# Optimization experiments

Hardware: AMD Instinct MI355X
Metric: run time of the kernel (lower is better)

Reference implementation:

```python
import jax, jax.numpy as jnp
import numpy as np

N, E = 50000, 600000
IN_C, HID, OUT_C = 256, 128, 2
R, B, L = 7, 8, 3
ALPHA = 0.1


def _rgcn(x, src, dst, etype, comp, basis, root, bias):
    # comp: [R,B], basis: [B,d,d] -> per-relation weights W: [R,d,d]
    n, d = x.shape
    W = jnp.einsum('rb,bdf->rdf', comp, basis)
    # combined (dst, relation) segment id for per-relation mean aggregation
    seg = dst * R + etype
    msg = x[src]  # [E,d] gather
    s = jax.ops.segment_sum(msg, seg, num_segments=n * R)  # [N*R,d]
    cnt = jax.ops.segment_sum(jnp.ones((E,), x.dtype), seg, num_segments=n * R)
    agg = (s / jnp.maximum(cnt, 1.0)[:, None]).reshape(n, R, d)  # per-relation mean
    return x @ root + bias + jnp.einsum('nrd,rdf->nf', agg, W)


def setup_inputs() -> dict:
    key = jax.random.key(0)
    ks = jax.random.split(key, 10)
    sc = 0.05
    x = jax.random.normal(ks[0], (N, IN_C), dtype=jnp.float32)
    edge_index = jax.random.randint(ks[1], (2, E), 0, N)
    edge_type = jax.random.randint(ks[2], (E,), 0, R)
    # GPR temp init: alpha*(1-alpha)^k, last entry (1-alpha)^K
    temp = jnp.asarray(ALPHA * (1.0 - ALPHA) ** np.arange(L + 1), dtype=jnp.float32)
    temp = temp.at[-1].set((1.0 - ALPHA) ** L)
    lin1_w = jax.random.normal(ks[3], (IN_C, HID), jnp.float32) * sc
    lin1_b = jnp.zeros((HID,), jnp.float32)
    lin2_w = jax.random.normal(ks[4], (HID, OUT_C), jnp.float32) * sc
    lin2_b = jnp.zeros((OUT_C,), jnp.float32)
    comps = jax.random.normal(ks[5], (L, R, B), jnp.float32) * sc
    bases = jax.random.normal(ks[6], (L, B, HID, HID), jnp.float32) * sc
    roots = jax.random.normal(ks[7], (L, HID, HID), jnp.float32) * sc
    conv_biases = jnp.zeros((L, HID), jnp.float32)
    return dict(x=x, edge_index=edge_index, edge_type=edge_type, temp=temp,
                lin1_w=lin1_w, lin1_b=lin1_b, lin2_w=lin2_w, lin2_b=lin2_b,
                comps=comps, bases=bases, roots=roots, conv_biases=conv_biases)


def reference(x, edge_index, edge_type, temp, lin1_w, lin1_b, lin2_w, lin2_b,
              comps, bases, roots, conv_biases):
    src, dst = edge_index[0], edge_index[1]
    h = x @ lin1_w + lin1_b
    hidden = h * temp[0]
    cur = hidden
    for i in range(L):
        cur = _rgcn(cur, src, dst, edge_type, comps[i], bases[i], roots[i], conv_biases[i])
        if i < L - 1:
            cur = jax.nn.relu(cur)  # dropout p=0.4 is identity in eval mode
        hidden = hidden + temp[i + 1] * cur
    return hidden @ lin2_w + lin2_b
```

## Files before the change

### kernel.cpp

```cpp
#include <hip/hip_runtime.h>
#include <cstdint>


constexpr int N_NODES  = 50000;
constexpr int E_EDGES  = 600000;
constexpr int R_REL    = 7;
constexpr int HID      = 128;
constexpr int IN_C     = 256;
constexpr int L_LAYERS = 3;
constexpr int AGG_COLS = 896;
constexpr int K_CAT    = 1024;
constexpr int NR       = N_NODES * R_REL;
constexpr int SCANR_BLOCKS = (NR + 255) / 256;

#define DEVI __device__ __forceinline__

using short8  = __attribute__((ext_vector_type(8))) short;
using floatx4 = __attribute__((ext_vector_type(4))) float;

DEVI unsigned short f2bf(float f) {
  unsigned u = __float_as_uint(f);
  unsigned r = (u + 0x7FFFu + ((u >> 16) & 1u)) >> 16;
  return (unsigned short)r;
}
DEVI float bf2f(unsigned short h) { return __uint_as_float(((unsigned)h) << 16); }

__global__ __launch_bounds__(256) void cast_x_kernel(
    const float* __restrict__ x, unsigned short* __restrict__ xbf)
{
  int i = blockIdx.x * 256 + threadIdx.x;
  if (i >= N_NODES * IN_C / 4) return;
  float4 v = ((const float4*)x)[i];
  uint2 p;
  p.x = (unsigned)f2bf(v.x) | ((unsigned)f2bf(v.y) << 16);
  p.y = (unsigned)f2bf(v.z) | ((unsigned)f2bf(v.w) << 16);
  ((uint2*)xbf)[i] = p;
}

__global__ __launch_bounds__(256) void cast_w1_kernel(
    const float* __restrict__ w1, unsigned short* __restrict__ w1T)
{
  int t = blockIdx.x * 256 + threadIdx.x;
  if (t >= HID * IN_C) return;
  int m = t >> 8, k = t & 255;
  w1T[m * IN_C + k] = f2bf(w1[k * HID + m]);
}

__global__ __launch_bounds__(256) void build_wcat2(
    const float* __restrict__ comps,
    const float* __restrict__ bases,
    const float* __restrict__ roots,
    unsigned short* __restrict__ wcat2T)
{
  int t = blockIdx.x * 256 + threadIdx.x;
  if (t >= L_LAYERS * 128 * K_CAT) return;
  int l   = t >> 17;
  int rem = t & 131071;
  int f   = rem >> 10;
  int k   = rem & 1023;
  float v;
  if (k < 128) {
    v = roots[((size_t)l * 128 + k) * 128 + f];
  } else {
    int r = (k - 128) >> 7, d = (k - 128) & 127;
    const float* cp = comps + ((size_t)l * R_REL + r) * 8;
    const float* bp = bases + (((size_t)l * 8) * 128 + d) * 128 + f;
    float s = 0.f;
#pragma unroll
    for (int b = 0; b < 8; ++b) s += cp[b] * bp[(size_t)b * 128 * 128];
    v = s;
  }
  wcat2T[t] = f2bf(v);
}

__global__ __launch_bounds__(256) void hist_kernel(
    const int* __restrict__ ei, const int* __restrict__ et,
    int* __restrict__ cntRel)
{
  int e = blockIdx.x * 256 + threadIdx.x;
  if (e >= E_EDGES) return;
  atomicAdd(&cntRel[ei[E_EDGES + e] * R_REL + et[e]], 1);
}

__global__ __launch_bounds__(256) void scanA_kernel(
    const int* __restrict__ cnt, int* __restrict__ tmpOff,
    int* __restrict__ blockSums)
{
  __shared__ int s[256];
  int i = blockIdx.x * 256 + threadIdx.x;
  int v = (i < NR) ? cnt[i] : 0;
  s[threadIdx.x] = v;
  __syncthreads();
#pragma unroll
  for (int d = 1; d < 256; d <<= 1) {
    int t = (threadIdx.x >= d) ? s[threadIdx.x - d] : 0;
    __syncthreads();
    s[threadIdx.x] += t;
    __syncthreads();
  }
  if (i < NR) tmpOff[i] = s[threadIdx.x] - v;
  if (threadIdx.x == 255) blockSums[blockIdx.x] = s[255];
}

__global__ __launch_bounds__(256) void scanB_kernel(int* __restrict__ bs)
{
  __shared__ int s[256];
  __shared__ int carry;
  if (threadIdx.x == 0) carry = 0;
  __syncthreads();
  for (int base = 0; base < SCANR_BLOCKS; base += 256) {
    int cOld = carry;
    int i = base + threadIdx.x;
    int v = (i < SCANR_BLOCKS) ? bs[i] : 0;
    s[threadIdx.x] = v;
    __syncthreads();
#pragma unroll
    for (int d = 1; d < 256; d <<= 1) {
      int t = (threadIdx.x >= d) ? s[threadIdx.x - d] : 0;
      __syncthreads();
      s[threadIdx.x] += t;
      __syncthreads();
    }
    if (i < SCANR_BLOCKS) bs[i] = s[threadIdx.x] - v + cOld;
    __syncthreads();
    if (threadIdx.x == 0) carry = cOld + s[255];
    __syncthreads();
  }
}

__global__ __launch_bounds__(256) void scanC_kernel(
    const int* __restrict__ tmpOff, const int* __restrict__ blockSums,
    int* __restrict__ drs)
{
  int i = blockIdx.x * 256 + threadIdx.x;
  if (i < NR) drs[i] = tmpOff[i] + blockSums[blockIdx.x];
  if (i == 0) drs[NR] = E_EDGES;
}

__global__ __launch_bounds__(256) void place_kernel(
    const int* __restrict__ ei, const int* __restrict__ et,
    const int* __restrict__ drs, int* __restrict__ cursor,
    unsigned short* __restrict__ esrc)
{
  int e = blockIdx.x * 256 + threadIdx.x;
  if (e >= E_EDGES) return;
  int seg = ei[E_EDGES + e] * R_REL + et[e];
  int pos = drs[seg] + atomicAdd(&cursor[seg], 1);
  esrc[pos] = (unsigned short)ei[e];
}

__global__ __launch_bounds__(256) void agg_reg_kernel(
    const unsigned short* __restrict__ curA,
    const unsigned short* __restrict__ esrc,
    const int* __restrict__ drs,
    unsigned short* __restrict__ aggB)
{
  const int tid  = threadIdx.x;
  const int lane = tid & 63;
  const int dst  = blockIdx.x * 4 + (tid >> 6);
  if (dst >= N_NODES) return;
  const int segBase = dst * R_REL;

  int bnd = drs[segBase + (lane & 7)];
  const int a0    = __shfl(bnd, 0);
  const int total = __shfl(bnd, 7) - a0;

  int pk = 0;
  if (lane < total) pk = (int)esrc[a0 + lane];

  const unsigned* colp = (const unsigned*)curA + lane;

  int p = a0;
  int aPrev = a0;
#pragma unroll
  for (int r = 0; r < R_REL; ++r) {
    int br = __shfl(bnd, r + 1);
    float sx = 0.f, sy = 0.f;
    for (; p < br; ++p) {
      int idx = p - a0;
      int src = (idx < 64) ? __shfl(pk, idx) : (int)esrc[p];
      unsigned v = colp[src * 64];
      sx += bf2f((unsigned short)(v & 0xFFFF));
      sy += bf2f((unsigned short)(v >> 16));
    }
    int c = br - aPrev;
    float sc = (c > 0) ? 1.0f / (float)c : 0.f;
    unsigned pck = (unsigned)f2bf(sx * sc) | ((unsigned)f2bf(sy * sc) << 16);
    *(unsigned*)(aggB + (size_t)dst * AGG_COLS + r * HID + lane * 2) = pck;
    aPrev = br;
  }
}

__global__ __launch_bounds__(256) void gemm_lin1(
    const unsigned short* __restrict__ A,
    const unsigned short* __restrict__ BT,
    const float* __restrict__ bias,
    const float* __restrict__ temp,
    float* __restrict__ out0,
    unsigned short* __restrict__ outT)
{
  __shared__ unsigned short As[128][136];
  __shared__ unsigned short Bs[128][136];
  const int tid  = threadIdx.x;
  const int row0 = blockIdx.x * 128;
  const int lane = tid & 63;
  const int wid  = tid >> 6;
  const int wrow = (wid & 1) * 64;
  const int wcol = (wid >> 1) * 64;
  const int l15  = lane & 15;
  const int quad = lane >> 4;

  floatx4 acc[4][4] = {};

  for (int k0 = 0; k0 < IN_C; k0 += 128) {
#pragma unroll
    for (int it = 0; it < 8; ++it) {
      int chunk = it * 256 + tid;
      int r = chunk >> 4, cc = (chunk & 15) << 3;
      int grow = row0 + r;
      uint4 va = make_uint4(0u, 0u, 0u, 0u);
      if (grow < N_NODES)
        va = *(const uint4*)(A + (size_t)grow * IN_C + k0 + cc);
      *(uint4*)(&As[r][cc]) = va;
      *(uint4*)(&Bs[r][cc]) = *(const uint4*)(BT + (size_t)r * IN_C + k0 + cc);
    }
    __syncthreads();
#pragma unroll
    for (int ks = 0; ks < 4; ++ks) {
      int kc = ks * 32 + quad * 8;
      short8 af[4], bfr[4];
#pragma unroll
      for (int i = 0; i < 4; ++i)
        af[i] = *(const short8*)(&As[wrow + i * 16 + l15][kc]);
#pragma unroll
      for (int j = 0; j < 4; ++j)
        bfr[j] = *(const short8*)(&Bs[wcol + j * 16 + l15][kc]);
#pragma unroll
      for (int i = 0; i < 4; ++i)
#pragma unroll
        for (int j = 0; j < 4; ++j)
          acc[i][j] = __builtin_amdgcn_mfma_f32_16x16x32_bf16(
              af[i], bfr[j], acc[i][j], 0, 0, 0);
    }
    __syncthreads();
  }

  float t0 = temp[0];
#pragma unroll
  for (int i = 0; i < 4; ++i) {
    int lrow0 = wrow + i * 16 + quad * 4;
#pragma unroll
    for (int j = 0; j < 4; ++j) {
      int gcol = wcol + j * 16 + l15;
      float bb = bias[gcol];
#pragma unroll
      for (int r = 0; r < 4; ++r) {
        float v = t0 * (acc[i][j][r] + bb);
        int grow = row0 + lrow0 + r;
        if (grow < N_NODES) out0[(size_t)grow * HID + gcol] = v;
        As[lrow0 + r][gcol] = f2bf(v);
      }
    }
  }
  __syncthreads();
#pragma unroll
  for (int it = 0; it < 8; ++it) {
    int chunk = it * 256 + tid;
    int r = chunk >> 4, cc = (chunk & 15) << 3;
    int grow = row0 + r;
    if (grow < N_NODES)
      *(uint4*)(outT + (size_t)grow * HID + cc) = *(const uint4*)(&As[r][cc]);
  }
}

__global__ __launch_bounds__(256) void gemm_layer(
    const unsigned short* __restrict__ curA,
    const unsigned short* __restrict__ aggB,
    const unsigned short* __restrict__ BT,
    const float* __restrict__ bias,
    const float* __restrict__ temp,
    float* __restrict__ hidden,
    unsigned short* __restrict__ curAout,
    int layer)
{
  __shared__ unsigned short Atile[64][136];
  __shared__ unsigned short Btile[128][136];
  const int tid  = threadIdx.x;
  const int row0 = blockIdx.x * 64;
  const int lane = tid & 63;
  const int wid  = tid >> 6;
  const int wrow = (wid & 1) * 32;
  const int wcol = (wid >> 1) * 64;
  const int l15  = lane & 15;
  const int quad = lane >> 4;

  floatx4 acc[2][4] = {};

  for (int p = 0; p < 8; ++p) {
#pragma unroll
    for (int it = 0; it < 8; ++it) {
      int chunk = it * 256 + tid;
      int n = chunk >> 4, cc = (chunk & 15) << 3;
      *(uint4*)(&Btile[n][cc]) =
          *(const uint4*)(BT + (size_t)n * K_CAT + p * 128 + cc);
    }
#pragma unroll
    for (int it = 0; it < 4; ++it) {
      int chunk = it * 256 + tid;
      int r = chunk >> 4, cc = (chunk & 15) << 3;
      int grow = row0 + r;
      uint4 va = make_uint4(0u, 0u, 0u, 0u);
      if (grow < N_NODES) {
        if (p == 0)
          va = *(const uint4*)(curA + (size_t)grow * HID + cc);
        else
          va = *(const uint4*)(aggB + (size_t)grow * AGG_COLS +
                               (p - 1) * 128 + cc);
      }
      *(uint4*)(&Atile[r][cc]) = va;
    }
    __syncthreads();
#pragma unroll
    for (int ks = 0; ks < 4; ++ks) {
      int kc = ks * 32 + quad * 8;
      short8 af[2], bfr[4];
#pragma unroll
      for (int i = 0; i < 2; ++i)
        af[i] = *(const short8*)(&Atile[wrow + i * 16 + l15][kc]);
#pragma unroll
      for (int j = 0; j < 4; ++j)
        bfr[j] = *(const short8*)(&Btile[wcol + j * 16 + l15][kc]);
#pragma unroll
      for (int i = 0; i < 2; ++i)
#pragma unroll
        for (int j = 0; j < 4; ++j)
          acc[i][j] = __builtin_amdgcn_mfma_f32_16x16x32_bf16(
              af[i], bfr[j], acc[i][j], 0, 0, 0);
    }
    __syncthreads();
  }

  const float tl = temp[layer + 1];
  const bool isLast = (layer == L_LAYERS - 1);
#pragma unroll
  for (int i = 0; i < 2; ++i) {
    int lrow0 = wrow + i * 16 + quad * 4;
#pragma unroll
    for (int j = 0; j < 4; ++j) {
      int gcol = wcol + j * 16 + l15;
      float bb = bias[gcol];
#pragma unroll
      for (int r = 0; r < 4; ++r) {
        int grow = row0 + lrow0 + r;
        float c = acc[i][j][r] + bb;
        if (!isLast) c = fmaxf(c, 0.f);
        if (grow < N_NODES) {
          float* hp = hidden + (size_t)grow * HID + gcol;
          *hp += tl * c;
        }
        Atile[lrow0 + r][gcol] = f2bf(c);
      }
    }
  }
  if (!isLast) {
    __syncthreads();
#pragma unroll
    for (int it = 0; it < 4; ++it) {
      int chunk = it * 256 + tid;
      int r = chunk >> 4, cc = (chunk & 15) << 3;
      int grow = row0 + r;
      if (grow < N_NODES)
        *(uint4*)(curAout + (size_t)grow * HID + cc) =
            *(const uint4*)(&Atile[r][cc]);
    }
  }
}

__global__ __launch_bounds__(256) void final_kernel(
    const float* __restrict__ hidden, const float* __restrict__ w2,
    const float* __restrict__ b2, float* __restrict__ out)
{
  int node = blockIdx.x * 4 + (threadIdx.x >> 6);
  int lane = threadIdx.x & 63;
  if (node >= N_NODES) return;
  float h0 = hidden[(size_t)node * HID + lane];
  float h1 = hidden[(size_t)node * HID + 64 + lane];
  float a0 = h0 * w2[lane * 2 + 0] + h1 * w2[(lane + 64) * 2 + 0];
  float a1 = h0 * w2[lane * 2 + 1] + h1 * w2[(lane + 64) * 2 + 1];
#pragma unroll
  for (int off = 32; off > 0; off >>= 1) {
    a0 += __shfl_down(a0, off);
    a1 += __shfl_down(a1, off);
  }
  if (lane == 0) {
    out[node * 2 + 0] = a0 + b2[0];
    out[node * 2 + 1] = a1 + b2[1];
  }
}

extern "C" void kernel_launch(void* const* d_in, const int* in_sizes, int n_in,
                              void* d_out, int out_size, void* d_ws, size_t ws_size,
                              hipStream_t stream) {
  const float* x     = (const float*)d_in[0];
  const int*   ei    = (const int*)d_in[1];
  const int*   et    = (const int*)d_in[2];
  const float* temp  = (const float*)d_in[3];
  const float* w1    = (const float*)d_in[4];
  const float* b1    = (const float*)d_in[5];
  const float* w2    = (const float*)d_in[6];
  const float* b2    = (const float*)d_in[7];
  const float* comps = (const float*)d_in[8];
  const float* bases = (const float*)d_in[9];
  const float* roots = (const float*)d_in[10];
  const float* cbias = (const float*)d_in[11];

  char* ws = (char*)d_ws;
  size_t off = 0;
  auto take = [&](size_t bytes) {
    char* p = ws + off;
    off = (off + bytes + 255) & ~(size_t)255;
    return p;
  };
  unsigned short* wcat2T = (unsigned short*)take((size_t)L_LAYERS * 128 * K_CAT * 2);
  unsigned short* xbf    = (unsigned short*)take((size_t)N_NODES * IN_C * 2);
  unsigned short* w1T    = (unsigned short*)take((size_t)HID * IN_C * 2);
  int*   cntRel  = (int*)take((size_t)NR * 4);
  int*   tmpOffR = (int*)take((size_t)NR * 4);
  int*   blockSumsR = (int*)take((size_t)SCANR_BLOCKS * 4);
  int*   drs     = (int*)take((size_t)(NR + 1) * 4);
  int*   cursorR = (int*)take((size_t)NR * 4);
  unsigned short* esrc = (unsigned short*)take((size_t)E_EDGES * 2);
  float* hidden  = (float*)take((size_t)N_NODES * HID * 4);
  unsigned short* curA  = (unsigned short*)take((size_t)N_NODES * HID * 2);
  unsigned short* curA2 = (unsigned short*)take((size_t)N_NODES * HID * 2);
  unsigned short* aggB  = (unsigned short*)take((size_t)N_NODES * AGG_COLS * 2);

  hipMemsetAsync(cntRel, 0, (size_t)NR * 4, stream);
  hipMemsetAsync(cursorR, 0, (size_t)NR * 4, stream);

  hipLaunchKernelGGL(build_wcat2, dim3((L_LAYERS * 128 * K_CAT + 255) / 256),
                     dim3(256), 0, stream, comps, bases, roots, wcat2T);
  hipLaunchKernelGGL(cast_x_kernel, dim3((N_NODES * IN_C / 4 + 255) / 256),
                     dim3(256), 0, stream, x, xbf);
  hipLaunchKernelGGL(cast_w1_kernel, dim3((HID * IN_C + 255) / 256), dim3(256),
                     0, stream, w1, w1T);
  hipLaunchKernelGGL(hist_kernel, dim3((E_EDGES + 255) / 256), dim3(256), 0,
                     stream, ei, et, cntRel);
  hipLaunchKernelGGL(scanA_kernel, dim3(SCANR_BLOCKS), dim3(256), 0, stream,
                     cntRel, tmpOffR, blockSumsR);
  hipLaunchKernelGGL(scanB_kernel, dim3(1), dim3(256), 0, stream, blockSumsR);
  hipLaunchKernelGGL(scanC_kernel, dim3(SCANR_BLOCKS), dim3(256), 0, stream,
                     tmpOffR, blockSumsR, drs);
  hipLaunchKernelGGL(place_kernel, dim3((E_EDGES + 255) / 256), dim3(256), 0,
                     stream, ei, et, drs, cursorR, esrc);

  const int rowBlocks   = (N_NODES + 127) / 128;
  const int rowBlocks64 = (N_NODES + 63) / 64;
  hipLaunchKernelGGL(gemm_lin1, dim3(rowBlocks), dim3(256), 0, stream,
                     xbf, w1T, b1, temp, hidden, curA);

  const unsigned short* cin = curA;
  unsigned short* cout = curA2;
  for (int l = 0; l < L_LAYERS; ++l) {
    hipLaunchKernelGGL(agg_reg_kernel, dim3((N_NODES + 3) / 4), dim3(256),
                       0, stream, cin, esrc, drs, aggB);
    hipLaunchKernelGGL(gemm_layer, dim3(rowBlocks64), dim3(256), 0, stream,
                       cin, aggB, wcat2T + (size_t)l * 128 * K_CAT,
                       cbias + (size_t)l * HID, temp, hidden, cout, l);
    const unsigned short* t = cin; cin = cout; cout = (unsigned short*)t;
  }

  hipLaunchKernelGGL(final_kernel, dim3((N_NODES + 3) / 4), dim3(256), 0, stream,
                     hidden, w2, b2, (float*)d_out);
}
```

Before: 587.7 us.

## Fuse x cast into lin1 GEMM and defer the hidden accumulation to the final kernel

```diff
diff --git a/kernel.cpp b/kernel.cpp
--- a/kernel.cpp
+++ b/kernel.cpp
@@ -24,18 +24,6 @@
   return (unsigned short)r;
 }
 DEVI float bf2f(unsigned short h) { return __uint_as_float(((unsigned)h) << 16); }
-
-__global__ __launch_bounds__(256) void cast_x_kernel(
-    const float* __restrict__ x, unsigned short* __restrict__ xbf)
-{
-  int i = blockIdx.x * 256 + threadIdx.x;
-  if (i >= N_NODES * IN_C / 4) return;
-  float4 v = ((const float4*)x)[i];
-  uint2 p;
-  p.x = (unsigned)f2bf(v.x) | ((unsigned)f2bf(v.y) << 16);
-  p.y = (unsigned)f2bf(v.z) | ((unsigned)f2bf(v.w) << 16);
-  ((uint2*)xbf)[i] = p;
-}
 
 __global__ __launch_bounds__(256) void cast_w1_kernel(
     const float* __restrict__ w1, unsigned short* __restrict__ w1T)
@@ -192,96 +180,11 @@
 }
 
 __global__ __launch_bounds__(256) void gemm_lin1(
-    const unsigned short* __restrict__ A,
+    const float* __restrict__ x,
     const unsigned short* __restrict__ BT,
     const float* __restrict__ bias,
     const float* __restrict__ temp,
-    float* __restrict__ out0,
-    unsigned short* __restrict__ outT)
-{
-  __shared__ unsigned short As[128][136];
-  __shared__ unsigned short Bs[128][136];
-  const int tid  = threadIdx.x;
-  const int row0 = blockIdx.x * 128;
-  const int lane = tid & 63;
-  const int wid  = tid >> 6;
-  const int wrow = (wid & 1) * 64;
-  const int wcol = (wid >> 1) * 64;
-  const int l15  = lane & 15;
-  const int quad = lane >> 4;
-
-  floatx4 acc[4][4] = {};
-
-  for (int k0 = 0; k0 < IN_C; k0 += 128) {
-#pragma unroll
-    for (int it = 0; it < 8; ++it) {
-      int chunk = it * 256 + tid;
-      int r = chunk >> 4, cc = (chunk & 15) << 3;
-      int grow = row0 + r;
-      uint4 va = make_uint4(0u, 0u, 0u, 0u);
-      if (grow < N_NODES)
-        va = *(const uint4*)(A + (size_t)grow * IN_C + k0 + cc);
-      *(uint4*)(&As[r][cc]) = va;
-      *(uint4*)(&Bs[r][cc]) = *(const uint4*)(BT + (size_t)r * IN_C + k0 + cc);
-    }
-    __syncthreads();
-#pragma unroll
-    for (int ks = 0; ks < 4; ++ks) {
-      int kc = ks * 32 + quad * 8;
-      short8 af[4], bfr[4];
-#pragma unroll
-      for (int i = 0; i < 4; ++i)
-        af[i] = *(const short8*)(&As[wrow + i * 16 + l15][kc]);
-#pragma unroll
-      for (int j = 0; j < 4; ++j)
-        bfr[j] = *(const short8*)(&Bs[wcol + j * 16 + l15][kc]);
-#pragma unroll
-      for (int i = 0; i < 4; ++i)
-#pragma unroll
-        for (int j = 0; j < 4; ++j)
-          acc[i][j] = __builtin_amdgcn_mfma_f32_16x16x32_bf16(
-              af[i], bfr[j], acc[i][j], 0, 0, 0);
-    }
-    __syncthreads();
-  }
-
-  float t0 = temp[0];
-#pragma unroll
-  for (int i = 0; i < 4; ++i) {
-    int lrow0 = wrow + i * 16 + quad * 4;
-#pragma unroll
-    for (int j = 0; j < 4; ++j) {
-      int gcol = wcol + j * 16 + l15;
-      float bb = bias[gcol];
-#pragma unroll
-      for (int r = 0; r < 4; ++r) {
-        float v = t0 * (acc[i][j][r] + bb);
-        int grow = row0 + lrow0 + r;
-        if (grow < N_NODES) out0[(size_t)grow * HID + gcol] = v;
-        As[lrow0 + r][gcol] = f2bf(v);
-      }
-    }
-  }
-  __syncthreads();
-#pragma unroll
-  for (int it = 0; it < 8; ++it) {
-    int chunk = it * 256 + tid;
-    int r = chunk >> 4, cc = (chunk & 15) << 3;
-    int grow = row0 + r;
-    if (grow < N_NODES)
-      *(uint4*)(outT + (size_t)grow * HID + cc) = *(const uint4*)(&As[r][cc]);
-  }
-}
-
-__global__ __launch_bounds__(256) void gemm_layer(
-    const unsigned short* __restrict__ curA,
-    const unsigned short* __restrict__ aggB,
-    const unsigned short* __restrict__ BT,
-    const float* __restrict__ bias,
-    const float* __restrict__ temp,
-    float* __restrict__ hidden,
-    unsigned short* __restrict__ curAout,
-    int layer)
+    unsigned short* __restrict__ b0out)
 {
   __shared__ unsigned short Atile[64][136];
   __shared__ unsigned short Btile[128][136];
@@ -296,6 +199,97 @@
 
   floatx4 acc[2][4] = {};
 
+  for (int k0 = 0; k0 < IN_C; k0 += 128) {
+#pragma unroll
+    for (int it = 0; it < 4; ++it) {
+      int chunk = it * 256 + tid;
+      int r = chunk >> 4, cc = (chunk & 15) << 3;
+      int grow = row0 + r;
+      uint4 va = make_uint4(0u, 0u, 0u, 0u);
+      if (grow < N_NODES) {
+        const float* xp = x + (size_t)grow * IN_C + k0 + cc;
+        float4 f0 = *(const float4*)xp;
+        float4 f1 = *(const float4*)(xp + 4);
+        va.x = (unsigned)f2bf(f0.x) | ((unsigned)f2bf(f0.y) << 16);
+        va.y = (unsigned)f2bf(f0.z) | ((unsigned)f2bf(f0.w) << 16);
+        va.z = (unsigned)f2bf(f1.x) | ((unsigned)f2bf(f1.y) << 16);
+        va.w = (unsigned)f2bf(f1.z) | ((unsigned)f2bf(f1.w) << 16);
+      }
+      *(uint4*)(&Atile[r][cc]) = va;
+    }
+#pragma unroll
+    for (int it = 0; it < 8; ++it) {
+      int chunk = it * 256 + tid;
+      int n = chunk >> 4, cc = (chunk & 15) << 3;
+      *(uint4*)(&Btile[n][cc]) =
+          *(const uint4*)(BT + (size_t)n * IN_C + k0 + cc);
+    }
+    __syncthreads();
+#pragma unroll
+    for (int ks = 0; ks < 4; ++ks) {
+      int kc = ks * 32 + quad * 8;
+      short8 af[2], bfr[4];
+#pragma unroll
+      for (int i = 0; i < 2; ++i)
+        af[i] = *(const short8*)(&Atile[wrow + i * 16 + l15][kc]);
+#pragma unroll
+      for (int j = 0; j < 4; ++j)
+        bfr[j] = *(const short8*)(&Btile[wcol + j * 16 + l15][kc]);
+#pragma unroll
+      for (int i = 0; i < 2; ++i)
+#pragma unroll
+        for (int j = 0; j < 4; ++j)
+          acc[i][j] = __builtin_amdgcn_mfma_f32_16x16x32_bf16(
+              af[i], bfr[j], acc[i][j], 0, 0, 0);
+    }
+    __syncthreads();
+  }
+
+  float t0 = temp[0];
+#pragma unroll
+  for (int i = 0; i < 2; ++i) {
+    int lrow0 = wrow + i * 16 + quad * 4;
+#pragma unroll
+    for (int j = 0; j < 4; ++j) {
+      int gcol = wcol + j * 16 + l15;
+      float bb = bias[gcol];
+#pragma unroll
+      for (int r = 0; r < 4; ++r)
+        Atile[lrow0 + r][gcol] = f2bf(t0 * (acc[i][j][r] + bb));
+    }
+  }
+  __syncthreads();
+#pragma unroll
+  for (int it = 0; it < 4; ++it) {
+    int chunk = it * 256 + tid;
+    int r = chunk >> 4, cc = (chunk & 15) << 3;
+    int grow = row0 + r;
+    if (grow < N_NODES)
+      *(uint4*)(b0out + (size_t)grow * HID + cc) = *(const uint4*)(&Atile[r][cc]);
+  }
+}
+
+__global__ __launch_bounds__(256) void gemm_layer(
+    const unsigned short* __restrict__ curA,
+    const unsigned short* __restrict__ aggB,
+    const unsigned short* __restrict__ BT,
+    const float* __restrict__ bias,
+    unsigned short* __restrict__ bout,
+    int layer)
+{
+  __shared__ unsigned short Atile[32][136];
+  __shared__ unsigned short Btile[128][136];
+  const int tid  = threadIdx.x;
+  const int row0 = blockIdx.x * 32;
+  const int lane = tid & 63;
+  const int wid  = tid >> 6;
+  const int wrow = (wid & 1) * 16;
+  const int wcol = (wid >> 1) * 64;
+  const int l15  = lane & 15;
+  const int quad = lane >> 4;
+
+  floatx4 acc[4] = {};
+
   for (int p = 0; p < 8; ++p) {
 #pragma unroll
     for (int it = 0; it < 8; ++it) {
@@ -305,7 +299,7 @@
           *(const uint4*)(BT + (size_t)n * K_CAT + p * 128 + cc);
     }
 #pragma unroll
-    for (int it = 0; it < 4; ++it) {
+    for (int it = 0; it < 2; ++it) {
       int chunk = it * 256 + tid;
       int r = chunk >> 4, cc = (chunk & 15) << 3;
       int grow = row0 + r;
@@ -323,78 +317,80 @@
 #pragma unroll
     for (int ks = 0; ks < 4; ++ks) {
       int kc = ks * 32 + quad * 8;
-      short8 af[2], bfr[4];
-#pragma unroll
-      for (int i = 0; i < 2; ++i)
-        af[i] = *(const short8*)(&Atile[wrow + i * 16 + l15][kc]);
+      short8 af = *(const short8*)(&Atile[wrow + l15][kc]);
+      short8 bfr[4];
 #pragma unroll
       for (int j = 0; j < 4; ++j)
         bfr[j] = *(const short8*)(&Btile[wcol + j * 16 + l15][kc]);
 #pragma unroll
-      for (int i = 0; i < 2; ++i)
-#pragma unroll
-        for (int j = 0; j < 4; ++j)
-          acc[i][j] = __builtin_amdgcn_mfma_f32_16x16x32_bf16(
-              af[i], bfr[j], acc[i][j], 0, 0, 0);
-    }
-    __syncthreads();
-  }
-
-  const float tl = temp[layer + 1];
+      for (int j = 0; j < 4; ++j)
+        acc[j] = __builtin_amdgcn_mfma_f32_16x16x32_bf16(af, bfr[j], acc[j],
+                                                         0, 0, 0);
+    }
+    __syncthreads();
+  }
+
   const bool isLast = (layer == L_LAYERS - 1);
-#pragma unroll
-  for (int i = 0; i < 2; ++i) {
-    int lrow0 = wrow + i * 16 + quad * 4;
+  {
+    int lrow0 = wrow + quad * 4;
 #pragma unroll
     for (int j = 0; j < 4; ++j) {
       int gcol = wcol + j * 16 + l15;
       float bb = bias[gcol];
 #pragma unroll
       for (int r = 0; r < 4; ++r) {
-        int grow = row0 + lrow0 + r;
-        float c = acc[i][j][r] + bb;
+        float c = acc[j][r] + bb;
         if (!isLast) c = fmaxf(c, 0.f);
-        if (grow < N_NODES) {
-          float* hp = hidden + (size_t)grow * HID + gcol;
-          *hp += tl * c;
-        }
         Atile[lrow0 + r][gcol] = f2bf(c);
       }
     }
   }
-  if (!isLast) {
-    __syncthreads();
-#pragma unroll
-    for (int it = 0; it < 4; ++it) {
-      int chunk = it * 256 + tid;
-      int r = chunk >> 4, cc = (chunk & 15) << 3;
-      int grow = row0 + r;
-      if (grow < N_NODES)
-        *(uint4*)(curAout + (size_t)grow * HID + cc) =
-            *(const uint4*)(&Atile[r][cc]);
-    }
+  __syncthreads();
+#pragma unroll
+  for (int it = 0; it < 2; ++it) {
+    int chunk = it * 256 + tid;
+    int r = chunk >> 4, cc = (chunk & 15) << 3;
+    int grow = row0 + r;
+    if (grow < N_NODES)
+      *(uint4*)(bout + (size_t)grow * HID + cc) = *(const uint4*)(&Atile[r][cc]);
   }
 }
 
 __global__ __launch_bounds__(256) void final_kernel(
-    const float* __restrict__ hidden, const float* __restrict__ w2,
-    const float* __restrict__ b2, float* __restrict__ out)
+    const unsigned short* __restrict__ b0, const unsigned short* __restrict__ b1,
+    const unsigned short* __restrict__ b2v, const unsigned short* __restrict__ b3,
+    const float* __restrict__ temp,
+    const float* __restrict__ w2, const float* __restrict__ b2bias,
+    float* __restrict__ out)
 {
   int node = blockIdx.x * 4 + (threadIdx.x >> 6);
   int lane = threadIdx.x & 63;
   if (node >= N_NODES) return;
-  float h0 = hidden[(size_t)node * HID + lane];
-  float h1 = hidden[(size_t)node * HID + 64 + lane];
-  float a0 = h0 * w2[lane * 2 + 0] + h1 * w2[(lane + 64) * 2 + 0];
-  float a1 = h0 * w2[lane * 2 + 1] + h1 * w2[(lane + 64) * 2 + 1];
+  float t1 = temp[1], t2 = temp[2], t3 = temp[3];
+  size_t base = (size_t)node * 64 + lane;
+  unsigned u0 = ((const unsigned*)b0)[base];
+  unsigned u1 = ((const unsigned*)b1)[base];
+  unsigned u2 = ((const unsigned*)b2v)[base];
+  unsigned u3 = ((const unsigned*)b3)[base];
+  float hx = bf2f((unsigned short)(u0 & 0xFFFF)) +
+             t1 * bf2f((unsigned short)(u1 & 0xFFFF)) +
+             t2 * bf2f((unsigned short)(u2 & 0xFFFF)) +
+             t3 * bf2f((unsigned short)(u3 & 0xFFFF));
+  float hy = bf2f((unsigned short)(u0 >> 16)) +
+             t1 * bf2f((unsigned short)(u1 >> 16)) +
+             t2 * bf2f((unsigned short)(u2 >> 16)) +
+             t3 * bf2f((unsigned short)(u3 >> 16));
+  int d0 = lane * 2, d1 = lane * 2 + 1;
+  float a0 = hx * w2[d0 * 2 + 0] + hy * w2[d1 * 2 + 0];
+  float a1 = hx * w2[d0 * 2 + 1] + hy * w2[d1 * 2 + 1];
 #pragma unroll
   for (int off = 32; off > 0; off >>= 1) {
     a0 += __shfl_down(a0, off);
     a1 += __shfl_down(a1, off);
   }
   if (lane == 0) {
-    out[node * 2 + 0] = a0 + b2[0];
-    out[node * 2 + 1] = a1 + b2[1];
+    out[node * 2 + 0] = a0 + b2bias[0];
+    out[node * 2 + 1] = a1 + b2bias[1];
   }
 }
 
@@ -422,7 +418,6 @@
     return p;
   };
   unsigned short* wcat2T = (unsigned short*)take((size_t)L_LAYERS * 128 * K_CAT * 2);
-  unsigned short* xbf    = (unsigned short*)take((size_t)N_NODES * IN_C * 2);
   unsigned short* w1T    = (unsigned short*)take((size_t)HID * IN_C * 2);
   int*   cntRel  = (int*)take((size_t)NR * 4);
   int*   tmpOffR = (int*)take((size_t)NR * 4);
@@ -430,18 +425,16 @@
   int*   drs     = (int*)take((size_t)(NR + 1) * 4);
   int*   cursorR = (int*)take((size_t)NR * 4);
   unsigned short* esrc = (unsigned short*)take((size_t)E_EDGES * 2);
-  float* hidden  = (float*)take((size_t)N_NODES * HID * 4);
-  unsigned short* curA  = (unsigned short*)take((size_t)N_NODES * HID * 2);
-  unsigned short* curA2 = (unsigned short*)take((size_t)N_NODES * HID * 2);
-  unsigned short* aggB  = (unsigned short*)take((size_t)N_NODES * AGG_COLS * 2);
+  unsigned short* bl[L_LAYERS + 1];
+  for (int i = 0; i <= L_LAYERS; ++i)
+    bl[i] = (unsigned short*)take((size_t)N_NODES * HID * 2);
+  unsigned short* aggB = (unsigned short*)take((size_t)N_NODES * AGG_COLS * 2);
 
   hipMemsetAsync(cntRel, 0, (size_t)NR * 4, stream);
   hipMemsetAsync(cursorR, 0, (size_t)NR * 4, stream);
 
   hipLaunchKernelGGL(build_wcat2, dim3((L_LAYERS * 128 * K_CAT + 255) / 256),
                      dim3(256), 0, stream, comps, bases, roots, wcat2T);
-  hipLaunchKernelGGL(cast_x_kernel, dim3((N_NODES * IN_C / 4 + 255) / 256),
-                     dim3(256), 0, stream, x, xbf);
   hipLaunchKernelGGL(cast_w1_kernel, dim3((HID * IN_C + 255) / 256), dim3(256),
                      0, stream, w1, w1T);
   hipLaunchKernelGGL(hist_kernel, dim3((E_EDGES + 255) / 256), dim3(256), 0,
@@ -454,22 +447,19 @@
   hipLaunchKernelGGL(place_kernel, dim3((E_EDGES + 255) / 256), dim3(256), 0,
                      stream, ei, et, drs, cursorR, esrc);
 
-  const int rowBlocks   = (N_NODES + 127) / 128;
   const int rowBlocks64 = (N_NODES + 63) / 64;
-  hipLaunchKernelGGL(gemm_lin1, dim3(rowBlocks), dim3(256), 0, stream,
-                     xbf, w1T, b1, temp, hidden, curA);
-
-  const unsigned short* cin = curA;
-  unsigned short* cout = curA2;
+  const int rowBlocks32 = (N_NODES + 31) / 32;
+  hipLaunchKernelGGL(gemm_lin1, dim3(rowBlocks64), dim3(256), 0, stream,
+                     x, w1T, b1, temp, bl[0]);
+
   for (int l = 0; l < L_LAYERS; ++l) {
     hipLaunchKernelGGL(agg_reg_kernel, dim3((N_NODES + 3) / 4), dim3(256),
-                       0, stream, cin, esrc, drs, aggB);
-    hipLaunchKernelGGL(gemm_layer, dim3(rowBlocks64), dim3(256), 0, stream,
-                       cin, aggB, wcat2T + (size_t)l * 128 * K_CAT,
-                       cbias + (size_t)l * HID, temp, hidden, cout, l);
-    const unsigned short* t = cin; cin = cout; cout = (unsigned short*)t;
+                       0, stream, bl[l], esrc, drs, aggB);
+    hipLaunchKernelGGL(gemm_layer, dim3(rowBlocks32), dim3(256), 0, stream,
+                       bl[l], aggB, wcat2T + (size_t)l * 128 * K_CAT,
+                       cbias + (size_t)l * HID, bl[l + 1], l);
   }
 
   hipLaunchKernelGGL(final_kernel, dim3((N_NODES + 3) / 4), dim3(256), 0, stream,
-                     hidden, w2, b2, (float*)d_out);
-}
+                     bl[0], bl[1], bl[2], bl[3], temp, w2, b2, (float*)d_out);
+}
```

Result: faster. 527.6 us (-10.2%).
